# Optimization experiments

Hardware: AMD Instinct MI355X
Metric: run time of the kernel (lower is better)

Reference implementation:

```python
import jax, jax.numpy as jnp
import numpy as np

B, T, D = 64, 512, 1024
H0, H1 = 1024, 1024

def setup_inputs() -> dict:
    key = jax.random.key(0)
    k1, k2, k3 = jax.random.split(key, 3)
    # scale weights ~ 1/sqrt(fan_in) so tanh doesn't saturate
    s0 = 1.0 / np.sqrt(H0 + D)
    s1 = 1.0 / np.sqrt(H1 + H0)
    return {
        "x": jax.random.normal(k1, (B, T, D), dtype=jnp.float32),
        "W0": jax.random.normal(k2, (H0 + D, H0), dtype=jnp.float32) * s0,
        "b0": jnp.zeros((H0,), dtype=jnp.float32),
        "W1": jax.random.normal(k3, (H1 + H0, H1), dtype=jnp.float32) * s1,
        "b1": jnp.zeros((H1,), dtype=jnp.float32),
    }

def reference(x, W0, b0, W1, b1):
    batch = x.shape[0]
    h0_init = jnp.zeros((batch, W0.shape[1]), dtype=x.dtype)
    h1_init = jnp.zeros((batch, W1.shape[1]), dtype=x.dtype)

    def step(carry, xt):
        h0, h1 = carry
        # layer 0: concat(prev hidden, input) -> dense -> tanh
        h0 = jnp.tanh(jnp.concatenate([h0, xt], axis=-1) @ W0 + b0)
        # layer 1 consumes layer 0 output
        h1 = jnp.tanh(jnp.concatenate([h1, h0], axis=-1) @ W1 + b1)
        return (h0, h1), h1

    xs = jnp.swapaxes(x, 0, 1)  # [T, B, D] time-major for scan
    (h0_f, h1_f), ys = jax.lax.scan(step, (h0_init, h1_init), xs)
    outputs = jnp.swapaxes(ys, 0, 1)  # [B, T, H1]
    final_state = jnp.concatenate([h0_f, h1_f], axis=-1)  # [B, H0+H1]
    return outputs, final_state
```

## Files before the change

kernel.cpp:

```cpp
#include <hip/hip_runtime.h>
#include <cmath>


typedef unsigned short u16;
typedef unsigned long long u64;
typedef __bf16 bf16x8 __attribute__((ext_vector_type(8)));
typedef u16    u16x8  __attribute__((ext_vector_type(8)));
typedef u16    u16x4  __attribute__((ext_vector_type(4)));
typedef float  f32x4  __attribute__((ext_vector_type(4)));

constexpr int BB = 64;
constexpr int TT = 512;
constexpr size_t SLOT   = (size_t)64 * 1024;
constexpr size_t SLAB_B = SLOT * 2;

constexpr size_t OFF_W0T = 262144;
constexpr size_t OFF_W1T = OFF_W0T + (size_t)1024 * 2048 * 2;
constexpr size_t OFF_R   = OFF_W1T + (size_t)1024 * 2048 * 2;

__device__ inline u16 f2bf(float f) {
  return __builtin_bit_cast(u16, (__bf16)f);
}
__device__ inline float bf2f(u16 v) {
  return (float)__builtin_bit_cast(__bf16, v);
}
__device__ inline float fast_tanh(float x) {
  x = fminf(15.f, fmaxf(-15.f, x));
  float e = __expf(2.f * x);
  return (e - 1.f) * __builtin_amdgcn_rcpf(e + 1.f);
}

__global__ void zero_flags(unsigned* f) {
  int i = blockIdx.x * 256 + threadIdx.x;
  if (i < 3 * 512 * 32) f[i] = 0;
}

__global__ void transpose_w(const float* __restrict__ W0,
                            const float* __restrict__ W1,
                            u16* __restrict__ wt_base) {
  __shared__ float tile[64][65];
  int bi  = blockIdx.x;
  int mat = bi >> 9;
  int t   = bi & 511;
  int tk = t & 31, tn = t >> 5;
  const float* W = mat ? W1 : W0;
  u16* Wt = wt_base + (size_t)mat * 1024 * 2048;
  int K0 = tk * 64, N0 = tn * 64;
  int tid = threadIdx.x;
  {
    int c4 = (tid & 15) * 4;
    int r  = tid >> 4;
    for (int i = 0; i < 4; ++i) {
      int kl = r + i * 16;
      float4 v = *(const float4*)(W + (size_t)(K0 + kl) * 1024 + N0 + c4);
      tile[kl][c4 + 0] = v.x; tile[kl][c4 + 1] = v.y;
      tile[kl][c4 + 2] = v.z; tile[kl][c4 + 3] = v.w;
    }
  }
  __syncthreads();
  {
    int nl = tid >> 3;
    int kc = (tid & 7) * 8;
    for (int pass = 0; pass < 2; ++pass) {
      int n = nl + pass * 32;
      u16x8 o;
      #pragma unroll
      for (int z = 0; z < 8; ++z) o[z] = f2bf(tile[kc + z][n]);
      *(u16x8*)(Wt + (size_t)(N0 + n) * 2048 + K0 + kc) = o;
    }
  }
}

__global__ void xconv(const float* __restrict__ x, u16* __restrict__ xb) {
  int bi = blockIdx.x;
  int b = bi >> 9, t = bi & 511;
  const float* src = x + ((size_t)b * TT + t) * 1024;
  u16* dst = xb + ((size_t)t * BB + b) * 1024;
  int i = threadIdx.x * 4;
  float4 v = *(const float4*)(src + i);
  u16x4 o; o[0] = f2bf(v.x); o[1] = f2bf(v.y); o[2] = f2bf(v.z); o[3] = f2bf(v.w);
  *(u16x4*)(dst + i) = o;
}

__device__ inline void poll1(unsigned* p) {
  while (__hip_atomic_load(p, __ATOMIC_RELAXED, __HIP_MEMORY_SCOPE_SYSTEM) == 0u)
    __builtin_amdgcn_s_sleep(1);
}

template<bool COHA>
__device__ inline void mm_core(const u16* Abase, const u16* bp, size_t aoff,
                               int q, int n15, f32x4& acc0, f32x4& acc1) {
  const u16* ap = Abase + aoff;
  #pragma unroll
  for (int ks = 0; ks < 32; ++ks) {
    bf16x8 a;
    if constexpr (COHA) {
      u64 lo = __hip_atomic_load((u64*)(ap + ks * 32),     __ATOMIC_RELAXED, __HIP_MEMORY_SCOPE_SYSTEM);
      u64 hi = __hip_atomic_load((u64*)(ap + ks * 32 + 4), __ATOMIC_RELAXED, __HIP_MEMORY_SCOPE_SYSTEM);
      union { u64 q2[2]; bf16x8 v; } un; un.q2[0] = lo; un.q2[1] = hi;
      a = un.v;
    } else {
      a = __builtin_bit_cast(bf16x8, *(const u16x8*)(ap + ks * 32));
    }
    int g = (4 * ks + q) ^ n15;
    bf16x8 b0 = __builtin_bit_cast(bf16x8, *(const u16x8*)(bp + g * 8));
    bf16x8 b1 = __builtin_bit_cast(bf16x8, *(const u16x8*)(bp + 16 * 1024 + g * 8));
    acc0 = __builtin_amdgcn_mfma_f32_16x16x32_bf16(a, b0, acc0, 0, 0, 0);
    acc1 = __builtin_amdgcn_mfma_f32_16x16x32_bf16(a, b1, acc1, 0, 0, 0);
  }
}
__device__ inline void mmf_core(const float* Ap, const u16* bp,
                                int q, int n15, f32x4& acc0, f32x4& acc1) {
  #pragma unroll
  for (int ks = 0; ks < 32; ++ks) {
    float4 v0 = *(const float4*)(Ap + ks * 32);
    float4 v1 = *(const float4*)(Ap + ks * 32 + 4);
    bf16x8 a;
    a[0]=(__bf16)v0.x; a[1]=(__bf16)v0.y; a[2]=(__bf16)v0.z; a[3]=(__bf16)v0.w;
    a[4]=(__bf16)v1.x; a[5]=(__bf16)v1.y; a[6]=(__bf16)v1.z; a[7]=(__bf16)v1.w;
    int g = (4 * ks + q) ^ n15;
    bf16x8 b0 = __builtin_bit_cast(bf16x8, *(const u16x8*)(bp + g * 8));
    bf16x8 b1 = __builtin_bit_cast(bf16x8, *(const u16x8*)(bp + 16 * 1024 + g * 8));
    acc0 = __builtin_amdgcn_mfma_f32_16x16x32_bf16(a, b0, acc0, 0, 0, 0);
    acc1 = __builtin_amdgcn_mfma_f32_16x16x32_bf16(a, b1, acc1, 0, 0, 0);
  }
}

template<bool COH>
__global__ void __launch_bounds__(256, 1)
rnn_seq(const float* __restrict__ x, const float* __restrict__ b0v,
        const float* __restrict__ b1v, float* __restrict__ out,
        unsigned* __restrict__ flags, const u16* __restrict__ W0t,
        const u16* __restrict__ W1t, u16* __restrict__ h0r,
        u16* __restrict__ h1r, u16* __restrict__ ur,
        const u16* __restrict__ xb, int use_xb) {
  constexpr int RMASK = COH ? 15 : 511;
  constexpr int UMASK = COH ? 31 : 511;
  constexpr int RING = 16, URING = 32;
  extern __shared__ u16 lds[];
  unsigned* fl_h0 = flags;
  unsigned* fl_h1 = flags + 512 * 32;
  unsigned* fl_u  = flags + 2 * 512 * 32;

  int wg = blockIdx.x, tid = threadIdx.x;
  int grp = wg >> 5, j = wg & 31;
  int n0 = j * 32;
  int lane = tid & 63, wave = tid >> 6;
  int n15 = lane & 15, q = lane >> 4;
  int r0 = wave * 16;

  {
    const u16* Wt = (grp == 1) ? W1t : W0t;
    int nh = (grp == 1) ? 2 : 1;
    for (int h = 0; h < nh; ++h) {
      int kb = (grp == 1) ? h * 1024 : (grp == 2 ? 1024 : 0);
      for (int idx = tid; idx < 32 * 128; idx += 256) {
        int n = idx >> 7, g = idx & 127;
        u16x8 v = *(const u16x8*)(Wt + (size_t)(n0 + n) * 2048 + kb + g * 8);
        *(u16x8*)(lds + h * 32768 + n * 1024 + ((g ^ (n & 15)) * 8)) = v;
      }
    }
  }
  __syncthreads();

  const size_t aoff = (size_t)(r0 + n15) * 1024 + q * 8;
  auto epi = [&](const f32x4& acc0, const f32x4& acc1, auto&& fn) {
    #pragma unroll
    for (int tile = 0; tile < 2; ++tile) {
      const f32x4& a = tile ? acc1 : acc0;
      int nn = n0 + n15 + tile * 16;
      #pragma unroll
      for (int i = 0; i < 4; ++i) fn(r0 + q * 4 + i, nn, a[i]);
    }
  };
  auto sc_store16 = [](u16* p, u16 v) {
    __hip_atomic_store(p, v, __ATOMIC_RELAXED, __HIP_MEMORY_SCOPE_SYSTEM);
  };

  const size_t FIN = (size_t)BB * TT * 1024;

  if (grp == 0) {
    for (int t = 0; t < TT; ++t) {
      if (tid < 32)      {                        poll1(&fl_u [t * 32 + tid]); }
      else if (tid < 64) { if (t > 0)             poll1(&fl_h0[(t - 1) * 32 + (tid - 32)]); }
      else if (tid < 96) { if (COH && t >= RING)  poll1(&fl_h1[(t - RING) * 32 + (tid - 64)]); }
      __syncthreads();
      f32x4 acc0 = {0.f, 0.f, 0.f, 0.f}, acc1 = acc0;
      if (t > 0)
        mm_core<COH>(h0r + (size_t)((t - 1) & RMASK) * SLOT, lds + n15 * 1024,
                     aoff, q, n15, acc0, acc1);
      u16* Uslab = ur + (size_t)(t & UMASK) * SLOT;
      u16* H = h0r + (size_t)(t & RMASK) * SLOT;
      epi(acc0, acc1, [&](int b, int nn, float a) {
        float uv = COH ? bf2f(__hip_atomic_load(&Uslab[b * 1024 + nn],
                              __ATOMIC_RELAXED, __HIP_MEMORY_SCOPE_SYSTEM))
                       : bf2f(Uslab[b * 1024 + nn]);
        float h = fast_tanh(a + uv);
        sc_store16(&H[b * 1024 + nn], f2bf(h));
        if (t == TT - 1)
          __builtin_nontemporal_store(h, &out[FIN + (size_t)b * 2048 + nn]);
      });
      __syncthreads();
      if (tid == 0)
        __hip_atomic_store(&fl_h0[t * 32 + j], 1u, __ATOMIC_RELAXED, __HIP_MEMORY_SCOPE_SYSTEM);
    }
  } else if (grp == 1) {
    for (int t = 0; t < TT; ++t) {
      if (tid < 32) poll1(&fl_h0[t * 32 + tid]);
      __syncthreads();
      f32x4 acc0 = {0.f, 0.f, 0.f, 0.f}, acc1 = acc0;
      mm_core<COH>(h0r + (size_t)(t & RMASK) * SLOT, lds + 32768 + n15 * 1024,
                   aoff, q, n15, acc0, acc1);
      if (t > 0) {
        if (tid < 32) poll1(&fl_h1[(t - 1) * 32 + tid]);
        __syncthreads();
        mm_core<COH>(h1r + (size_t)((t - 1) & RMASK) * SLOT, lds + n15 * 1024,
                     aoff, q, n15, acc0, acc1);
      }
      u16* H = h1r + (size_t)(t & RMASK) * SLOT;
      epi(acc0, acc1, [&](int b, int nn, float a) {
        float h = fast_tanh(a + b1v[nn]);
        sc_store16(&H[b * 1024 + nn], f2bf(h));
        __builtin_nontemporal_store(h, &out[((size_t)b * TT + t) * 1024 + nn]);
        if (t == TT - 1)
          __builtin_nontemporal_store(h, &out[FIN + (size_t)b * 2048 + 1024 + nn]);
      });
      __syncthreads();
      if (tid == 0)
        __hip_atomic_store(&fl_h1[t * 32 + j], 1u, __ATOMIC_RELAXED, __HIP_MEMORY_SCOPE_SYSTEM);
    }
  } else {
    for (int t = 0; t < TT; ++t) {
      if (COH && t >= URING) {
        if (tid < 32) poll1(&fl_h0[(t - URING) * 32 + tid]);
        __syncthreads();
      }
      f32x4 acc0 = {0.f, 0.f, 0.f, 0.f}, acc1 = acc0;
      if (use_xb) {
        mm_core<false>(xb + (size_t)t * SLOT, lds + n15 * 1024,
                       aoff, q, n15, acc0, acc1);
      } else {
        const float* Ap = x + ((size_t)(r0 + n15) * TT + t) * 1024 + q * 8;
        mmf_core(Ap, lds + n15 * 1024, q, n15, acc0, acc1);
      }
      u16* U = ur + (size_t)(t & UMASK) * SLOT;
      epi(acc0, acc1, [&](int b, int nn, float a) {
        sc_store16(&U[b * 1024 + nn], f2bf(a + b0v[nn]));
      });
      __syncthreads();
      if (tid == 0)
        __hip_atomic_store(&fl_u[t * 32 + j], 1u, __ATOMIC_RELAXED, __HIP_MEMORY_SCOPE_SYSTEM);
    }
  }
}

extern "C" void kernel_launch(void* const* d_in, const int* in_sizes, int n_in,
                              void* d_out, int out_size, void* d_ws, size_t ws_size,
                              hipStream_t stream) {
  const float* x  = (const float*)d_in[0];
  const float* W0 = (const float*)d_in[1];
  const float* b0 = (const float*)d_in[2];
  const float* W1 = (const float*)d_in[3];
  const float* b1 = (const float*)d_in[4];
  float* out = (float*)d_out;
  unsigned char* ws = (unsigned char*)d_ws;

  const size_t WS_PLAIN = OFF_R + 4ull * 512 * SLAB_B;
  bool plain = ws_size >= WS_PLAIN;
  size_t nslot  = plain ? 512 : 16;
  size_t nuslot = plain ? 512 : 32;
  size_t o_h0 = OFF_R;
  size_t o_h1 = o_h0 + nslot  * SLAB_B;
  size_t o_u  = o_h1 + nslot  * SLAB_B;
  size_t o_xb = o_u  + nuslot * SLAB_B;
  int use_xb = (plain || ws_size >= o_xb + (size_t)TT * SLAB_B) ? 1 : 0;

  unsigned* flags = (unsigned*)ws;
  const u16* W0t = (const u16*)(ws + OFF_W0T);
  const u16* W1t = (const u16*)(ws + OFF_W1T);
  u16* h0r = (u16*)(ws + o_h0);
  u16* h1r = (u16*)(ws + o_h1);
  u16* ur  = (u16*)(ws + o_u);
  u16* xb  = (u16*)(ws + o_xb);

  zero_flags<<<192, 256, 0, stream>>>(flags);
  transpose_w<<<1024, 256, 0, stream>>>(W0, W1, (u16*)(ws + OFF_W0T));
  if (use_xb) xconv<<<32768, 256, 0, stream>>>(x, xb);

  (void)hipFuncSetAttribute((const void*)rnn_seq<false>,
                            hipFuncAttributeMaxDynamicSharedMemorySize, 131072);
  (void)hipFuncSetAttribute((const void*)rnn_seq<true>,
                            hipFuncAttributeMaxDynamicSharedMemorySize, 131072);

  void* args[12];
  args[0]  = (void*)&x;    args[1]  = (void*)&b0;   args[2]  = (void*)&b1;
  args[3]  = (void*)&out;  args[4]  = (void*)&flags;
  args[5]  = (void*)&W0t;  args[6]  = (void*)&W1t;
  args[7]  = (void*)&h0r;  args[8]  = (void*)&h1r;  args[9]  = (void*)&ur;
  args[10] = (void*)&xb;   args[11] = (void*)&use_xb;
  hipLaunchCooperativeKernel(plain ? (void*)rnn_seq<false> : (void*)rnn_seq<true>,
                             dim3(96), dim3(256), args, 131072, stream);
}
```

Measured before the change: 5.389 ms.

## Split K across 16 waves per block with LDS reduction and staged ring stores

Each workgroup grows from 4 to 16 waves. The K dimension of each per-step matmul is split four ways, so each wave runs 8 MFMA k-steps instead of 32, and partial sums are combined through an LDS scratch buffer. Results are staged in LDS as a bf16 tile and written to the ring with coalesced 32-bit atomic stores, and the U values are prefetched into LDS. The goal is to shorten the latency-bound serial critical path of each timestep, at the cost of extra barriers, more LDS, and a larger shared-memory request.

```diff
diff --git a/kernel.cpp b/kernel.cpp
--- a/kernel.cpp
+++ b/kernel.cpp
@@ -3,6 +3,7 @@
 
 
 typedef unsigned short u16;
+typedef unsigned int   u32;
 typedef unsigned long long u64;
 typedef __bf16 bf16x8 __attribute__((ext_vector_type(8)));
 typedef u16    u16x8  __attribute__((ext_vector_type(8)));
@@ -18,12 +19,10 @@
 constexpr size_t OFF_W1T = OFF_W0T + (size_t)1024 * 2048 * 2;
 constexpr size_t OFF_R   = OFF_W1T + (size_t)1024 * 2048 * 2;
 
-__device__ inline u16 f2bf(float f) {
-  return __builtin_bit_cast(u16, (__bf16)f);
-}
-__device__ inline float bf2f(u16 v) {
-  return (float)__builtin_bit_cast(__bf16, v);
-}
+constexpr int LDS_REQ = 159744;
+
+__device__ inline u16 f2bf(float f) { return __builtin_bit_cast(u16, (__bf16)f); }
+__device__ inline float bf2f(u16 v) { return (float)__builtin_bit_cast(__bf16, v); }
 __device__ inline float fast_tanh(float x) {
   x = fminf(15.f, fmaxf(-15.f, x));
   float e = __expf(2.f * x);
@@ -88,11 +87,11 @@
 }
 
 template<bool COHA>
-__device__ inline void mm_core(const u16* Abase, const u16* bp, size_t aoff,
-                               int q, int n15, f32x4& acc0, f32x4& acc1) {
+__device__ inline void mm8(const u16* Abase, const u16* bp, size_t aoff,
+                           int gbase, int n15, f32x4& acc0, f32x4& acc1) {
   const u16* ap = Abase + aoff;
   #pragma unroll
-  for (int ks = 0; ks < 32; ++ks) {
+  for (int ks = 0; ks < 8; ++ks) {
     bf16x8 a;
     if constexpr (COHA) {
       u64 lo = __hip_atomic_load((u64*)(ap + ks * 32),     __ATOMIC_RELAXED, __HIP_MEMORY_SCOPE_SYSTEM);
@@ -102,23 +101,23 @@
     } else {
       a = __builtin_bit_cast(bf16x8, *(const u16x8*)(ap + ks * 32));
     }
-    int g = (4 * ks + q) ^ n15;
+    int g = (gbase + 4 * ks) ^ n15;
     bf16x8 b0 = __builtin_bit_cast(bf16x8, *(const u16x8*)(bp + g * 8));
     bf16x8 b1 = __builtin_bit_cast(bf16x8, *(const u16x8*)(bp + 16 * 1024 + g * 8));
     acc0 = __builtin_amdgcn_mfma_f32_16x16x32_bf16(a, b0, acc0, 0, 0, 0);
     acc1 = __builtin_amdgcn_mfma_f32_16x16x32_bf16(a, b1, acc1, 0, 0, 0);
   }
 }
-__device__ inline void mmf_core(const float* Ap, const u16* bp,
-                                int q, int n15, f32x4& acc0, f32x4& acc1) {
+__device__ inline void mmf8(const float* Ap, const u16* bp,
+                            int gbase, int n15, f32x4& acc0, f32x4& acc1) {
   #pragma unroll
-  for (int ks = 0; ks < 32; ++ks) {
+  for (int ks = 0; ks < 8; ++ks) {
     float4 v0 = *(const float4*)(Ap + ks * 32);
     float4 v1 = *(const float4*)(Ap + ks * 32 + 4);
     bf16x8 a;
     a[0]=(__bf16)v0.x; a[1]=(__bf16)v0.y; a[2]=(__bf16)v0.z; a[3]=(__bf16)v0.w;
     a[4]=(__bf16)v1.x; a[5]=(__bf16)v1.y; a[6]=(__bf16)v1.z; a[7]=(__bf16)v1.w;
-    int g = (4 * ks + q) ^ n15;
+    int g = (gbase + 4 * ks) ^ n15;
     bf16x8 b0 = __builtin_bit_cast(bf16x8, *(const u16x8*)(bp + g * 8));
     bf16x8 b1 = __builtin_bit_cast(bf16x8, *(const u16x8*)(bp + 16 * 1024 + g * 8));
     acc0 = __builtin_amdgcn_mfma_f32_16x16x32_bf16(a, b0, acc0, 0, 0, 0);
@@ -127,7 +126,7 @@
 }
 
 template<bool COH>
-__global__ void __launch_bounds__(256, 1)
+__global__ void __launch_bounds__(1024, 1)
 rnn_seq(const float* __restrict__ x, const float* __restrict__ b0v,
         const float* __restrict__ b1v, float* __restrict__ out,
         unsigned* __restrict__ flags, const u16* __restrict__ W0t,
@@ -146,107 +145,178 @@
   int grp = wg >> 5, j = wg & 31;
   int n0 = j * 32;
   int lane = tid & 63, wave = tid >> 6;
+  int rb = wave & 3, ksl = wave >> 2;
   int n15 = lane & 15, q = lane >> 4;
-  int r0 = wave * 16;
+  int r0 = rb * 16;
+
+  u16*   wlds = lds;
+  float* scr  = (float*)((char*)lds + ((grp == 1) ? 131072 : 65536));
+  u16*   hch  = (u16*)((char*)scr + 24576);
+  u32*   uc   = (u32*)((char*)hch + 4096);
 
   {
     const u16* Wt = (grp == 1) ? W1t : W0t;
     int nh = (grp == 1) ? 2 : 1;
     for (int h = 0; h < nh; ++h) {
       int kb = (grp == 1) ? h * 1024 : (grp == 2 ? 1024 : 0);
-      for (int idx = tid; idx < 32 * 128; idx += 256) {
+      for (int idx = tid; idx < 32 * 128; idx += 1024) {
         int n = idx >> 7, g = idx & 127;
         u16x8 v = *(const u16x8*)(Wt + (size_t)(n0 + n) * 2048 + kb + g * 8);
-        *(u16x8*)(lds + h * 32768 + n * 1024 + ((g ^ (n & 15)) * 8)) = v;
+        *(u16x8*)(wlds + h * 32768 + n * 1024 + ((g ^ (n & 15)) * 8)) = v;
       }
     }
   }
   __syncthreads();
 
-  const size_t aoff = (size_t)(r0 + n15) * 1024 + q * 8;
-  auto epi = [&](const f32x4& acc0, const f32x4& acc1, auto&& fn) {
+  const size_t aoff = (size_t)(r0 + n15) * 1024 + ksl * 256 + q * 8;
+  const int gbase = 32 * ksl + q;
+  const u16* bp0 = wlds + n15 * 1024;
+  const u16* bp1 = wlds + 32768 + n15 * 1024;
+
+  float bia = 0.f, bib = 0.f;
+  if (grp == 1) { bia = b1v[n0 + n15]; bib = b1v[n0 + n15 + 16]; }
+  if (grp == 2) { bia = b0v[n0 + n15]; bib = b0v[n0 + n15 + 16]; }
+
+  auto scr_write = [&](const f32x4& a0, const f32x4& a1) {
+    int base = ((rb * 3 + ksl - 1) * 2) * 256 + (q * 4) * 16 + n15;
     #pragma unroll
-    for (int tile = 0; tile < 2; ++tile) {
-      const f32x4& a = tile ? acc1 : acc0;
-      int nn = n0 + n15 + tile * 16;
+    for (int i = 0; i < 4; ++i) scr[base + i * 16] = a0[i];
+    #pragma unroll
+    for (int i = 0; i < 4; ++i) scr[base + 256 + i * 16] = a1[i];
+  };
+  auto scr_sum = [&](f32x4& a0, f32x4& a1) {
+    #pragma unroll
+    for (int s = 0; s < 3; ++s) {
+      int base = ((rb * 3 + s) * 2) * 256 + (q * 4) * 16 + n15;
       #pragma unroll
-      for (int i = 0; i < 4; ++i) fn(r0 + q * 4 + i, nn, a[i]);
+      for (int i = 0; i < 4; ++i) a0[i] += scr[base + i * 16];
+      #pragma unroll
+      for (int i = 0; i < 4; ++i) a1[i] += scr[base + 256 + i * 16];
     }
   };
-  auto sc_store16 = [](u16* p, u16 v) {
-    __hip_atomic_store(p, v, __ATOMIC_RELAXED, __HIP_MEMORY_SCOPE_SYSTEM);
+  auto hch_write = [&](const f32x4& a0, const f32x4& a1, auto&& act) {
+    #pragma unroll
+    for (int i = 0; i < 4; ++i) {
+      int b = r0 + q * 4 + i;
+      hch[b * 32 + n15]      = f2bf(act(a0[i], 0));
+      hch[b * 32 + n15 + 16] = f2bf(act(a1[i], 1));
+    }
+  };
+  const int sb  = tid >> 4;
+  const int scc = (tid & 15) * 2;
+  auto ring_store = [&](u16* slab) {
+    u32 v = ((u32*)hch)[tid];
+    __hip_atomic_store((u32*)(slab + sb * 1024 + n0 + scc), v,
+                       __ATOMIC_RELAXED, __HIP_MEMORY_SCOPE_SYSTEM);
   };
 
   const size_t FIN = (size_t)BB * TT * 1024;
 
   if (grp == 0) {
     for (int t = 0; t < TT; ++t) {
-      if (tid < 32)      {                        poll1(&fl_u [t * 32 + tid]); }
-      else if (tid < 64) { if (t > 0)             poll1(&fl_h0[(t - 1) * 32 + (tid - 32)]); }
-      else if (tid < 96) { if (COH && t >= RING)  poll1(&fl_h1[(t - RING) * 32 + (tid - 64)]); }
+      if (tid < 32)      { if (t > 0)            poll1(&fl_h0[(t - 1) * 32 + tid]); }
+      else if (tid < 64) {                       poll1(&fl_u [t * 32 + (tid - 32)]); }
+      else if (tid < 96) { if (COH && t >= RING) poll1(&fl_h1[(t - RING) * 32 + (tid - 64)]); }
       __syncthreads();
       f32x4 acc0 = {0.f, 0.f, 0.f, 0.f}, acc1 = acc0;
       if (t > 0)
-        mm_core<COH>(h0r + (size_t)((t - 1) & RMASK) * SLOT, lds + n15 * 1024,
-                     aoff, q, n15, acc0, acc1);
-      u16* Uslab = ur + (size_t)(t & UMASK) * SLOT;
-      u16* H = h0r + (size_t)(t & RMASK) * SLOT;
-      epi(acc0, acc1, [&](int b, int nn, float a) {
-        float uv = COH ? bf2f(__hip_atomic_load(&Uslab[b * 1024 + nn],
-                              __ATOMIC_RELAXED, __HIP_MEMORY_SCOPE_SYSTEM))
-                       : bf2f(Uslab[b * 1024 + nn]);
-        float h = fast_tanh(a + uv);
-        sc_store16(&H[b * 1024 + nn], f2bf(h));
-        if (t == TT - 1)
-          __builtin_nontemporal_store(h, &out[FIN + (size_t)b * 2048 + nn]);
-      });
+        mm8<COH>(h0r + (size_t)((t - 1) & RMASK) * SLOT, bp0, aoff, gbase, n15, acc0, acc1);
+      {
+        const u16* us = ur + (size_t)(t & UMASK) * SLOT;
+        const u32* up = (const u32*)(us + sb * 1024 + n0 + scc);
+        u32 v = COH ? __hip_atomic_load((u32*)up, __ATOMIC_RELAXED, __HIP_MEMORY_SCOPE_SYSTEM)
+                    : *up;
+        uc[tid] = v;
+      }
+      if (ksl > 0) scr_write(acc0, acc1);
+      __syncthreads();
+      if (ksl == 0) {
+        scr_sum(acc0, acc1);
+        hch_write(acc0, acc1, [&](float a, int tile) {
+          int b = 0; (void)b;
+          return a;
+        });
+        #pragma unroll
+        for (int i = 0; i < 4; ++i) {
+          int b = r0 + q * 4 + i;
+          float u0 = bf2f(((u16*)uc)[b * 32 + n15]);
+          float u1 = bf2f(((u16*)uc)[b * 32 + n15 + 16]);
+          hch[b * 32 + n15]      = f2bf(fast_tanh(acc0[i] + u0));
+          hch[b * 32 + n15 + 16] = f2bf(fast_tanh(acc1[i] + u1));
+        }
+      }
+      __syncthreads();
+      ring_store(h0r + (size_t)(t & RMASK) * SLOT);
       __syncthreads();
       if (tid == 0)
         __hip_atomic_store(&fl_h0[t * 32 + j], 1u, __ATOMIC_RELAXED, __HIP_MEMORY_SCOPE_SYSTEM);
+      if (t == TT - 1) {
+        u32 v = ((u32*)hch)[tid];
+        float2 o; o.x = bf2f((u16)(v & 0xffff)); o.y = bf2f((u16)(v >> 16));
+        *(float2*)&out[FIN + (size_t)sb * 2048 + n0 + scc] = o;
+      }
     }
   } else if (grp == 1) {
     for (int t = 0; t < TT; ++t) {
       if (tid < 32) poll1(&fl_h0[t * 32 + tid]);
       __syncthreads();
       f32x4 acc0 = {0.f, 0.f, 0.f, 0.f}, acc1 = acc0;
-      mm_core<COH>(h0r + (size_t)(t & RMASK) * SLOT, lds + 32768 + n15 * 1024,
-                   aoff, q, n15, acc0, acc1);
-      if (t > 0) {
-        if (tid < 32) poll1(&fl_h1[(t - 1) * 32 + tid]);
-        __syncthreads();
-        mm_core<COH>(h1r + (size_t)((t - 1) & RMASK) * SLOT, lds + n15 * 1024,
-                     aoff, q, n15, acc0, acc1);
-      }
-      u16* H = h1r + (size_t)(t & RMASK) * SLOT;
-      epi(acc0, acc1, [&](int b, int nn, float a) {
-        float h = fast_tanh(a + b1v[nn]);
-        sc_store16(&H[b * 1024 + nn], f2bf(h));
-        __builtin_nontemporal_store(h, &out[((size_t)b * TT + t) * 1024 + nn]);
-        if (t == TT - 1)
-          __builtin_nontemporal_store(h, &out[FIN + (size_t)b * 2048 + 1024 + nn]);
-      });
+      mm8<COH>(h0r + (size_t)(t & RMASK) * SLOT, bp1, aoff, gbase, n15, acc0, acc1);
+      if (tid < 32 && t > 0) poll1(&fl_h1[(t - 1) * 32 + tid]);
+      __syncthreads();
+      if (t > 0)
+        mm8<COH>(h1r + (size_t)((t - 1) & RMASK) * SLOT, bp0, aoff, gbase, n15, acc0, acc1);
+      if (ksl > 0) scr_write(acc0, acc1);
+      __syncthreads();
+      if (ksl == 0) {
+        scr_sum(acc0, acc1);
+        #pragma unroll
+        for (int i = 0; i < 4; ++i) {
+          int b = r0 + q * 4 + i;
+          hch[b * 32 + n15]      = f2bf(fast_tanh(acc0[i] + bia));
+          hch[b * 32 + n15 + 16] = f2bf(fast_tanh(acc1[i] + bib));
+        }
+      }
+      __syncthreads();
+      ring_store(h1r + (size_t)(t & RMASK) * SLOT);
       __syncthreads();
       if (tid == 0)
         __hip_atomic_store(&fl_h1[t * 32 + j], 1u, __ATOMIC_RELAXED, __HIP_MEMORY_SCOPE_SYSTEM);
+      {
+        u32 v = ((u32*)hch)[tid];
+        float2 o; o.x = bf2f((u16)(v & 0xffff)); o.y = bf2f((u16)(v >> 16));
+        __builtin_nontemporal_store(o.x, &out[((size_t)sb * TT + t) * 1024 + n0 + scc]);
+        __builtin_nontemporal_store(o.y, &out[((size_t)sb * TT + t) * 1024 + n0 + scc + 1]);
+        if (t == TT - 1)
+          *(float2*)&out[FIN + (size_t)sb * 2048 + 1024 + n0 + scc] = o;
+      }
     }
   } else {
     for (int t = 0; t < TT; ++t) {
       if (COH && t >= URING) {
         if (tid < 32) poll1(&fl_h0[(t - URING) * 32 + tid]);
-        __syncthreads();
-      }
+      }
+      __syncthreads();
       f32x4 acc0 = {0.f, 0.f, 0.f, 0.f}, acc1 = acc0;
       if (use_xb) {
-        mm_core<false>(xb + (size_t)t * SLOT, lds + n15 * 1024,
-                       aoff, q, n15, acc0, acc1);
+        mm8<false>(xb + (size_t)t * SLOT, bp0, aoff, gbase, n15, acc0, acc1);
       } else {
-        const float* Ap = x + ((size_t)(r0 + n15) * TT + t) * 1024 + q * 8;
-        mmf_core(Ap, lds + n15 * 1024, q, n15, acc0, acc1);
-      }
-      u16* U = ur + (size_t)(t & UMASK) * SLOT;
-      epi(acc0, acc1, [&](int b, int nn, float a) {
-        sc_store16(&U[b * 1024 + nn], f2bf(a + b0v[nn]));
-      });
+        const float* Ap = x + ((size_t)(r0 + n15) * TT + t) * 1024 + ksl * 256 + q * 8;
+        mmf8(Ap, bp0, gbase, n15, acc0, acc1);
+      }
+      if (ksl > 0) scr_write(acc0, acc1);
+      __syncthreads();
+      if (ksl == 0) {
+        scr_sum(acc0, acc1);
+        #pragma unroll
+        for (int i = 0; i < 4; ++i) {
+          int b = r0 + q * 4 + i;
+          hch[b * 32 + n15]      = f2bf(acc0[i] + bia);
+          hch[b * 32 + n15 + 16] = f2bf(acc1[i] + bib);
+        }
+      }
+      __syncthreads();
+      ring_store(ur + (size_t)(t & UMASK) * SLOT);
       __syncthreads();
       if (tid == 0)
         __hip_atomic_store(&fl_u[t * 32 + j], 1u, __ATOMIC_RELAXED, __HIP_MEMORY_SCOPE_SYSTEM);
@@ -288,9 +358,9 @@
   if (use_xb) xconv<<<32768, 256, 0, stream>>>(x, xb);
 
   (void)hipFuncSetAttribute((const void*)rnn_seq<false>,
-                            hipFuncAttributeMaxDynamicSharedMemorySize, 131072);
+                            hipFuncAttributeMaxDynamicSharedMemorySize, LDS_REQ);
   (void)hipFuncSetAttribute((const void*)rnn_seq<true>,
-                            hipFuncAttributeMaxDynamicSharedMemorySize, 131072);
+                            hipFuncAttributeMaxDynamicSharedMemorySize, LDS_REQ);
 
   void* args[12];
   args[0]  = (void*)&x;    args[1]  = (void*)&b0;   args[2]  = (void*)&b1;
@@ -299,5 +369,5 @@
   args[7]  = (void*)&h0r;  args[8]  = (void*)&h1r;  args[9]  = (void*)&ur;
   args[10] = (void*)&xb;   args[11] = (void*)&use_xb;
   hipLaunchCooperativeKernel(plain ? (void*)rnn_seq<false> : (void*)rnn_seq<true>,
-                             dim3(96), dim3(256), args, 131072, stream);
-}
+                             dim3(96), dim3(1024), args, LDS_REQ, stream);
+}
```

Result: faster. 4.642 ms (-13.9%).
